# Optimization experiments

Hardware: AMD Instinct MI355X
Metric: run time of the kernel (lower is better)

## Reference

```python
import jax, jax.numpy as jnp
import numpy as np

NV = 100000   # vehicle nodes
NE = 100000   # 'edge' nodes (dst type)
E = 250000    # graph edges (connects relation)
VDIM = 16
EDIM = 16
HID = 128
HEADS = 4
DH = 128      # out_feats per head (GATv2Conv(hid, hid))
EPS = 1e-5
NEG_SLOPE = 0.2


def _layernorm(x, g, b):
    mu = x.mean(-1, keepdims=True)
    var = ((x - mu) ** 2).mean(-1, keepdims=True)
    return (x - mu) * jax.lax.rsqrt(var + EPS) * g + b


def setup_inputs() -> dict:
    key = jax.random.key(0)
    ks = jax.random.split(key, 20)
    s = 0.05
    return {
        "v_feat": jax.random.normal(ks[0], (NV, VDIM), jnp.float32),
        "e_feat": jax.random.normal(ks[1], (NE, EDIM), jnp.float32),
        "Wv": jax.random.normal(ks[2], (VDIM, HID), jnp.float32) * s,
        "bv": jnp.zeros((HID,), jnp.float32),
        "gv": jnp.ones((HID,), jnp.float32),
        "betav": jnp.zeros((HID,), jnp.float32),
        "We": jax.random.normal(ks[3], (EDIM, HID), jnp.float32) * s,
        "be": jnp.zeros((HID,), jnp.float32),
        "ge": jnp.ones((HID,), jnp.float32),
        "betae": jnp.zeros((HID,), jnp.float32),
        "Wsrc": jax.random.normal(ks[4], (HID, HEADS * DH), jnp.float32) * s,
        "bsrc": jnp.zeros((HEADS * DH,), jnp.float32),
        "Wdst": jax.random.normal(ks[5], (HID, HEADS * DH), jnp.float32) * s,
        "bdst": jnp.zeros((HEADS * DH,), jnp.float32),
        "attn": jax.random.normal(ks[6], (HEADS, DH), jnp.float32) * s,
        "Wp": jax.random.normal(ks[7], (HID, HID), jnp.float32) * s,
        "bp": jnp.zeros((HID,), jnp.float32),
        "src": jax.random.randint(ks[8], (E,), 0, NV, jnp.int32),
        "dst": jax.random.randint(ks[9], (E,), 0, NE, jnp.int32),
    }


def reference(v_feat, e_feat, Wv, bv, gv, betav, We, be, ge, betae,
              Wsrc, bsrc, Wdst, bdst, attn, Wp, bp, src, dst):
    # --- node-type encoders: Linear -> ReLU -> LayerNorm ---
    h_v = _layernorm(jax.nn.relu(v_feat @ Wv + bv), gv, betav)      # [NV, HID]
    h_e = _layernorm(jax.nn.relu(e_feat @ We + be), ge, betae)      # [NE, HID]

    # --- GATv2Conv (bipartite: vehicle -> edge), 4 heads ---
    fs = (h_v @ Wsrc + bsrc).reshape(NV, HEADS, DH)                 # src proj
    fd = (h_e @ Wdst + bdst).reshape(NE, HEADS, DH)                 # dst proj
    e = jax.nn.leaky_relu(fs[src] + fd[dst], NEG_SLOPE)             # [E, H, D]
    score = jnp.einsum("ehd,hd->eh", e, attn)                       # [E, H]
    # segment-wise (per-dst-node) softmax over incoming edges
    smax = jax.ops.segment_max(score, dst, num_segments=NE)         # [NE, H]
    ex = jnp.exp(score - smax[dst])
    denom = jax.ops.segment_sum(ex, dst, num_segments=NE)
    alpha = ex / denom[dst]                                         # [E, H]
    out = jax.ops.segment_sum(alpha[:, :, None] * fs[src], dst,
                              num_segments=NE)                      # [NE, H, D]

    # HeteroGraphConv mean-aggregate (single relation -> identity),
    # then mean over heads (edge_out.dim()==3 branch)
    edge_out = out.mean(axis=1)                                     # [NE, HID]

    # feature_proj: Linear -> ReLU -> Dropout(eval: identity)
    return jax.nn.relu(edge_out @ Wp + bp)
```

## Files before the change

kernel.cpp:

```cpp
#include <hip/hip_runtime.h>
#include <hip/hip_bf16.h>
#include <math.h>

#define NV 100000
#define NE_N 100000
#define NEDGE 250000
#define NEG 0.2f
#define LN_EPS 1e-5f

typedef __bf16 bf16_t;
typedef __bf16 bf16x8 __attribute__((ext_vector_type(8)));
typedef float f32x4 __attribute__((ext_vector_type(4)));

__device__ inline unsigned short f2bfu(float f) {
    return __builtin_bit_cast(unsigned short, (__bf16)f);
}
__device__ inline float bfu2f(unsigned short u) {
    return (float)__builtin_bit_cast(__bf16, u);
}
__device__ inline float blo(unsigned w) { return __uint_as_float(w << 16); }
__device__ inline float bhi(unsigned w) { return __uint_as_float(w & 0xffff0000u); }
__device__ inline float lrelu(float x) { return x > 0.f ? x : NEG * x; }
__device__ inline unsigned pk2(float a, float b) {
    return (unsigned)f2bfu(a) | ((unsigned)f2bfu(b) << 16);
}

__global__ __launch_bounds__(256) void prep_kernel(
    const float* __restrict__ Wsrc, const float* __restrict__ Wdst,
    const float* __restrict__ Wp, bf16_t* __restrict__ pS,
    bf16_t* __restrict__ pD, bf16_t* __restrict__ pP)
{
    int t = blockIdx.x * 256 + threadIdx.x;
    if (t < 8192) {
        int ksq = t >> 9, col = t & 511;
#pragma unroll
        for (int j = 0; j < 8; ++j)
            pS[(size_t)t * 8 + j] = (bf16_t)Wsrc[(ksq * 8 + j) * 512 + col];
    } else if (t < 16384) {
        int g = t - 8192;
        int ksq = g >> 9, col = g & 511;
#pragma unroll
        for (int j = 0; j < 8; ++j)
            pD[(size_t)g * 8 + j] = (bf16_t)Wdst[(ksq * 8 + j) * 512 + col];
    } else if (t < 18432) {
        int g = t - 16384;
        int ksq = g >> 7, col = g & 127;
#pragma unroll
        for (int j = 0; j < 8; ++j)
            pP[(size_t)g * 8 + j] = (bf16_t)Wp[(ksq * 8 + j) * 128 + col];
    }
}

__global__ __launch_bounds__(256) void count_kernel(
    const int* __restrict__ dst, int* __restrict__ deg)
{
    int t = blockIdx.x * 256 + threadIdx.x;
    if (t < NEDGE) atomicAdd(&deg[dst[t]], 1);
}

__global__ __launch_bounds__(256) void scan1_kernel(
    const int* __restrict__ deg, int* __restrict__ offs, int* __restrict__ bsum)
{
    __shared__ int s[256];
    int i = blockIdx.x * 256 + threadIdx.x;
    int v = (i < NE_N) ? deg[i] : 0;
    s[threadIdx.x] = v;
    __syncthreads();
    for (int off = 1; off < 256; off <<= 1) {
        int t_ = (threadIdx.x >= off) ? s[threadIdx.x - off] : 0;
        __syncthreads();
        s[threadIdx.x] += t_;
        __syncthreads();
    }
    if (i < NE_N) offs[i] = s[threadIdx.x] - v;
    if (threadIdx.x == 255) bsum[blockIdx.x] = s[255];
}

__global__ __launch_bounds__(512) void scan2_kernel(int* __restrict__ bsum, int nb)
{
    __shared__ int s[512];
    int t = threadIdx.x;
    int v = (t < nb) ? bsum[t] : 0;
    s[t] = v;
    __syncthreads();
    for (int off = 1; off < 512; off <<= 1) {
        int t_ = (t >= off) ? s[t - off] : 0;
        __syncthreads();
        s[t] += t_;
        __syncthreads();
    }
    if (t < nb) bsum[t] = s[t] - v;
}

__global__ __launch_bounds__(256) void scan3_kernel(
    int* __restrict__ offs, const int* __restrict__ bsum, int* __restrict__ cursor)
{
    int i = blockIdx.x * 256 + threadIdx.x;
    if (i < NE_N) {
        int o = offs[i] + bsum[blockIdx.x];
        offs[i] = o;
        cursor[i] = o;
    }
}

__global__ __launch_bounds__(256) void scatter_kernel(
    const int* __restrict__ dst, int* __restrict__ cursor, int* __restrict__ eidx)
{
    int t = blockIdx.x * 256 + threadIdx.x;
    if (t < NEDGE) {
        int pos = atomicAdd(&cursor[dst[t]], 1);
        eidx[pos] = t;
    }
}

__global__ __launch_bounds__(256, 4) void enc_proj_kernel(
    const float* __restrict__ featV, const float* __restrict__ WencV,
    const float* __restrict__ bencV, const float* __restrict__ gV,
    const float* __restrict__ betaV, const bf16_t* __restrict__ ApackV,
    const float* __restrict__ bprojV, unsigned short* __restrict__ outV,
    const float* __restrict__ featE, const float* __restrict__ WencE,
    const float* __restrict__ bencE, const float* __restrict__ gE,
    const float* __restrict__ betaE, const bf16_t* __restrict__ ApackE,
    const float* __restrict__ bprojE, unsigned short* __restrict__ outE,
    int nblk1, int M)
{
    __shared__ unsigned short Hs[64 * 136];

    int b = blockIdx.x;
    bool isV = b < nblk1;
    const float* feat  = isV ? featV  : featE;
    const float* Wenc  = isV ? WencV  : WencE;
    const float* benc  = isV ? bencV  : bencE;
    const float* gln   = isV ? gV     : gE;
    const float* beta  = isV ? betaV  : betaE;
    const bf16_t* Apack = isV ? ApackV : ApackE;
    const float* bproj = isV ? bprojV : bprojE;
    unsigned short* out = isV ? outV : outE;
    int row0 = (isV ? b : b - nblk1) * 64;

    int t = threadIdx.x;
    int l = t & 63;
    int w = t >> 6;
    int rbase = __builtin_amdgcn_readfirstlane(w * 16);

    float wc0[16], wc1[16];
#pragma unroll
    for (int k = 0; k < 16; ++k) {
        float2 wv = *(const float2*)(Wenc + k * 128 + 2 * l);
        wc0[k] = wv.x;
        wc1[k] = wv.y;
    }
    float2 bv2 = *(const float2*)(benc + 2 * l);

#pragma unroll
    for (int i = 0; i < 16; ++i) {
        int grow = row0 + rbase + i;
        if (grow >= M) grow = M - 1;
        const float* fr = feat + (size_t)grow * 16;
        float a0 = bv2.x, a1 = bv2.y;
#pragma unroll
        for (int k = 0; k < 16; ++k) {
            float f = fr[k];
            a0 = fmaf(f, wc0[k], a0);
            a1 = fmaf(f, wc1[k], a1);
        }
        a0 = fmaxf(a0, 0.f);
        a1 = fmaxf(a1, 0.f);
        *(unsigned*)&Hs[(rbase + i) * 136 + 2 * l] = pk2(a0, a1);
    }

    float s = 0.f, s2 = 0.f;
    {
        int rr = rbase + (l >> 2);
        int q = l & 3;
#pragma unroll
        for (int j = 0; j < 4; ++j) {
            uint4 v = *(const uint4*)&Hs[rr * 136 + q * 32 + j * 8];
            float x;
            x = blo(v.x); s += x; s2 = fmaf(x, x, s2);
            x = bhi(v.x); s += x; s2 = fmaf(x, x, s2);
            x = blo(v.y); s += x; s2 = fmaf(x, x, s2);
            x = bhi(v.y); s += x; s2 = fmaf(x, x, s2);
            x = blo(v.z); s += x; s2 = fmaf(x, x, s2);
            x = bhi(v.z); s += x; s2 = fmaf(x, x, s2);
            x = blo(v.w); s += x; s2 = fmaf(x, x, s2);
            x = bhi(v.w); s += x; s2 = fmaf(x, x, s2);
        }
    }
    s  += __shfl_xor(s, 1, 64);  s  += __shfl_xor(s, 2, 64);
    s2 += __shfl_xor(s2, 1, 64); s2 += __shfl_xor(s2, 2, 64);
    float mu  = s * (1.f / 128.f);
    float var = s2 * (1.f / 128.f) - mu * mu;
    float inv = rsqrtf(var + LN_EPS);

    int kq = l >> 4;
    int ln = l & 15;
    float mu_r  = __shfl(mu,  ln * 4, 64);
    float inv_r = __shfl(inv, ln * 4, 64);

    bf16x8 bfr[4];
#pragma unroll
    for (int ks = 0; ks < 4; ++ks) {
        int c0 = ks * 32 + kq * 8;
        uint4 v = *(const uint4*)&Hs[(rbase + ln) * 136 + c0];
        float4 g0 = *(const float4*)(gln + c0);
        float4 g1 = *(const float4*)(gln + c0 + 4);
        float4 b0 = *(const float4*)(beta + c0);
        float4 b1 = *(const float4*)(beta + c0 + 4);
        uint4 p;
        p.x = pk2(fmaf((blo(v.x) - mu_r) * inv_r, g0.x, b0.x),
                  fmaf((bhi(v.x) - mu_r) * inv_r, g0.y, b0.y));
        p.y = pk2(fmaf((blo(v.y) - mu_r) * inv_r, g0.z, b0.z),
                  fmaf((bhi(v.y) - mu_r) * inv_r, g0.w, b0.w));
        p.z = pk2(fmaf((blo(v.z) - mu_r) * inv_r, g1.x, b1.x),
                  fmaf((bhi(v.z) - mu_r) * inv_r, g1.y, b1.y));
        p.w = pk2(fmaf((blo(v.w) - mu_r) * inv_r, g1.z, b1.z),
                  fmaf((bhi(v.w) - mu_r) * inv_r, g1.w, b1.w));
        bfr[ks] = __builtin_bit_cast(bf16x8, p);
    }

    unsigned short* stag = Hs + rbase * 136;
    int node = row0 + rbase + ln;
    bool wr = node < M;

    bf16x8 a_cur[4], a_nxt[4];
#pragma unroll
    for (int ks = 0; ks < 4; ++ks)
        a_cur[ks] = *(const bf16x8*)(Apack + ((size_t)(ks * 4 + kq) * 512 + ln) * 8);

#pragma unroll
    for (int pass = 0; pass < 4; ++pass) {
        int colp = pass * 128;
#pragma unroll
        for (int mt = 0; mt < 8; ++mt) {
            int nidx = pass * 8 + mt + 1;
            if (nidx < 32) {
                int ncol = (nidx >> 3) * 128 + (nidx & 7) * 16 + ln;
#pragma unroll
                for (int ks = 0; ks < 4; ++ks)
                    a_nxt[ks] = *(const bf16x8*)(Apack + ((size_t)(ks * 4 + kq) * 512 + ncol) * 8);
            }

            f32x4 acc = {0.f, 0.f, 0.f, 0.f};
#pragma unroll
            for (int ks = 0; ks < 4; ++ks)
                acc = __builtin_amdgcn_mfma_f32_16x16x32_bf16(a_cur[ks], bfr[ks], acc, 0, 0, 0);

            int col = colp + mt * 16 + kq * 4;
            float4 bb = *(const float4*)(bproj + col);
            ushort4 o;
            o.x = f2bfu(acc[0] + bb.x);
            o.y = f2bfu(acc[1] + bb.y);
            o.z = f2bfu(acc[2] + bb.z);
            o.w = f2bfu(acc[3] + bb.w);
            *(ushort4*)&stag[ln * 136 + mt * 16 + kq * 4] = o;

#pragma unroll
            for (int ks = 0; ks < 4; ++ks)
                a_cur[ks] = a_nxt[ks];
        }
#pragma unroll
        for (int i = 0; i < 4; ++i) {
            uint4 v = *(const uint4*)&stag[ln * 136 + i * 32 + kq * 8];
            if (wr)
                *(uint4*)(out + (size_t)node * 512 + colp + i * 32 + kq * 8) = v;
        }
    }
}

__global__ __launch_bounds__(256) void final_gemm_kernel(
    const float* __restrict__ A, const bf16_t* __restrict__ Ppack,
    const float* __restrict__ bp, float* __restrict__ C, int M)
{
    __shared__ unsigned short Hs[64 * 136];
    int t = threadIdx.x;
    int lane = t & 63;
    int w = t >> 6;
    int row0 = blockIdx.x * 64;

#pragma unroll
    for (int i = 0; i < 8; ++i) {
        int f4 = i * 256 + t;
        int r = f4 >> 5;
        int c4 = (f4 & 31) * 4;
        float4 v = make_float4(0.f, 0.f, 0.f, 0.f);
        if (row0 + r < M)
            v = ((const float4*)(A + (size_t)(row0 + r) * 128))[f4 & 31];
        ushort4 o;
        o.x = f2bfu(v.x); o.y = f2bfu(v.y); o.z = f2bfu(v.z); o.w = f2bfu(v.w);
        *(ushort4*)&Hs[r * 136 + c4] = o;
    }
    __syncthreads();

    int kq = lane >> 4;
    int ln = lane & 15;

    f32x4 acc[2][4];
#pragma unroll
    for (int mt = 0; mt < 2; ++mt)
#pragma unroll
        for (int nt = 0; nt < 4; ++nt) {
            f32x4 z = {0.f, 0.f, 0.f, 0.f};
            acc[mt][nt] = z;
        }

#pragma unroll
    for (int ks = 0; ks < 4; ++ks) {
        bf16x8 bfr[4];
#pragma unroll
        for (int nt = 0; nt < 4; ++nt) {
            const uint4* p = (const uint4*)&Hs[(nt * 16 + ln) * 136 + ks * 32 + kq * 8];
            bfr[nt] = __builtin_bit_cast(bf16x8, *p);
        }
        bf16x8 afr[2];
#pragma unroll
        for (int mt = 0; mt < 2; ++mt) {
            int colA = w * 32 + mt * 16 + ln;
            afr[mt] = *(const bf16x8*)(Ppack + ((size_t)(ks * 4 + kq) * 128 + colA) * 8);
        }
#pragma unroll
        for (int mt = 0; mt < 2; ++mt)
#pragma unroll
            for (int nt = 0; nt < 4; ++nt)
                acc[mt][nt] = __builtin_amdgcn_mfma_f32_16x16x32_bf16(
                    afr[mt], bfr[nt], acc[mt][nt], 0, 0, 0);
    }

#pragma unroll
    for (int mt = 0; mt < 2; ++mt) {
        int col = w * 32 + mt * 16 + kq * 4;
        float4 bb = *(const float4*)(bp + col);
#pragma unroll
        for (int nt = 0; nt < 4; ++nt) {
            int node = row0 + nt * 16 + ln;
            if (node < M) {
                float4 o;
                o.x = fmaxf(acc[mt][nt][0] + bb.x, 0.f);
                o.y = fmaxf(acc[mt][nt][1] + bb.y, 0.f);
                o.z = fmaxf(acc[mt][nt][2] + bb.z, 0.f);
                o.w = fmaxf(acc[mt][nt][3] + bb.w, 0.f);
                *(float4*)(C + (size_t)node * 128 + col) = o;
            }
        }
    }
}

__global__ __launch_bounds__(256) void softagg_kernel(
    const unsigned short* __restrict__ fs, const unsigned short* __restrict__ fdp,
    const float* __restrict__ attn, const int* __restrict__ src,
    const int* __restrict__ offs, const int* __restrict__ deg,
    const int* __restrict__ eidx, float* __restrict__ out)
{
    int d = blockIdx.x * 4 + (threadIdx.x >> 6);
    if (d >= NE_N) return;
    int l = threadIdx.x & 63;
    int r0 = offs[d];
    int n = deg[d];
    int o = l * 8;

    uint4 fv = *(const uint4*)(fdp + (size_t)d * 512 + o);
    float fdv[8] = { blo(fv.x), bhi(fv.x), blo(fv.y), bhi(fv.y),
                     blo(fv.z), bhi(fv.z), blo(fv.w), bhi(fv.w) };
    float4 w0 = *(const float4*)(attn + o);
    float4 w1 = *(const float4*)(attn + o + 4);
    float wv[8] = { w0.x, w0.y, w0.z, w0.w, w1.x, w1.y, w1.z, w1.w };

    float m = -1e30f, sm = 0.f;
    float acc[8];
#pragma unroll
    for (int j = 0; j < 8; ++j) acc[j] = 0.f;

    for (int base = 0; base < n; base += 64) {
        int cnt = min(n - base, 64);
        int sl = 0;
        if (l < cnt) sl = src[eidx[r0 + base + l]];
        for (int i = 0; i < cnt; ++i) {
            int s = __shfl(sl, i, 64);
            uint4 a = *(const uint4*)(fs + (size_t)s * 512 + o);
            float fsv[8] = { blo(a.x), bhi(a.x), blo(a.y), bhi(a.y),
                             blo(a.z), bhi(a.z), blo(a.w), bhi(a.w) };
            float p = 0.f;
#pragma unroll
            for (int j = 0; j < 8; ++j)
                p = fmaf(lrelu(fsv[j] + fdv[j]), wv[j], p);
#pragma unroll
            for (int mk = 1; mk < 16; mk <<= 1)
                p += __shfl_xor(p, mk, 64);
            float mn = fmaxf(m, p);
            float c  = __expf(m - mn);
            float av = __expf(p - mn);
            sm = sm * c + av;
            m = mn;
#pragma unroll
            for (int j = 0; j < 8; ++j)
                acc[j] = fmaf(av, fsv[j], acc[j] * c);
        }
    }

    float inv = (n > 0) ? 0.25f / sm : 0.f;
#pragma unroll
    for (int j = 0; j < 8; ++j) {
        float v = acc[j] * inv;
        v += __shfl_xor(v, 16, 64);
        v += __shfl_xor(v, 32, 64);
        acc[j] = v;
    }
    if (l < 16) {
        float4 o0 = make_float4(acc[0], acc[1], acc[2], acc[3]);
        float4 o1 = make_float4(acc[4], acc[5], acc[6], acc[7]);
        *(float4*)(out + (size_t)d * 128 + l * 8) = o0;
        *(float4*)(out + (size_t)d * 128 + l * 8 + 4) = o1;
    }
}

extern "C" void kernel_launch(void* const* d_in, const int* in_sizes, int n_in,
                              void* d_out, int out_size, void* d_ws, size_t ws_size,
                              hipStream_t stream)
{
    const float* v_feat = (const float*)d_in[0];
    const float* e_feat = (const float*)d_in[1];
    const float* Wv     = (const float*)d_in[2];
    const float* bv     = (const float*)d_in[3];
    const float* gv     = (const float*)d_in[4];
    const float* betav  = (const float*)d_in[5];
    const float* We     = (const float*)d_in[6];
    const float* be     = (const float*)d_in[7];
    const float* ge     = (const float*)d_in[8];
    const float* betae  = (const float*)d_in[9];
    const float* Wsrc   = (const float*)d_in[10];
    const float* bsrc   = (const float*)d_in[11];
    const float* Wdst   = (const float*)d_in[12];
    const float* bdst   = (const float*)d_in[13];
    const float* attn   = (const float*)d_in[14];
    const float* Wp     = (const float*)d_in[15];
    const float* bp     = (const float*)d_in[16];
    const int*   src    = (const int*)d_in[17];
    const int*   dst    = (const int*)d_in[18];
    float* out = (float*)d_out;

    unsigned short* fs = (unsigned short*)d_ws;
    unsigned short* fd = fs + (size_t)NV * 512;
    int* deg    = (int*)(fd + (size_t)NE_N * 512);
    int* offs   = deg + NE_N;
    int* cursor = offs + NE_N;
    int* bsum   = cursor + NE_N;
    int* eidx   = bsum + 512;
    bf16_t* pS  = (bf16_t*)(eidx + NEDGE);
    bf16_t* pD  = pS + 65536;
    bf16_t* pP  = pD + 65536;

    const int NB_SCAN = (NE_N + 255) / 256;

    prep_kernel<<<72, 256, 0, stream>>>(Wsrc, Wdst, Wp, pS, pD, pP);

    hipMemsetAsync(deg, 0, (size_t)NE_N * sizeof(int), stream);
    count_kernel<<<(NEDGE + 255) / 256, 256, 0, stream>>>(dst, deg);
    scan1_kernel<<<NB_SCAN, 256, 0, stream>>>(deg, offs, bsum);
    scan2_kernel<<<1, 512, 0, stream>>>(bsum, NB_SCAN);
    scan3_kernel<<<NB_SCAN, 256, 0, stream>>>(offs, bsum, cursor);
    scatter_kernel<<<(NEDGE + 255) / 256, 256, 0, stream>>>(dst, cursor, eidx);

    enc_proj_kernel<<<3126, 256, 0, stream>>>(
        v_feat, Wv, bv, gv, betav, pS, bsrc, fs,
        e_feat, We, be, ge, betae, pD, bdst, fd,
        1563, 100000);

    softagg_kernel<<<NE_N / 4, 256, 0, stream>>>(fs, fd, attn, src, offs, deg,
                                                 eidx, out);

    final_gemm_kernel<<<1563, 256, 0, stream>>>(out, pP, bp, out, NE_N);
}
```

Measured before the change: 334.8 us.

## Restructure encoder-projection kernel to single-wave blocks processing 32 rows each

The encoder+projection kernel changes from 4-wave blocks, where each wave handles 16 rows, to 1-wave blocks where the wave handles 32 rows as two 16-row MFMA tiles. Each loaded weight fragment (Apack) now feeds two MFMAs, halving the weight-fragment global loads per row, and the LayerNorm reduction is reorganised to two lanes per row. The trade-off is more blocks, fewer waves per block, more registers per wave (two B-fragment sets and accumulators), and a longer serial encoder loop per wave, which may reduce latency hiding.

```diff
diff --git a/kernel.cpp b/kernel.cpp
--- a/kernel.cpp
+++ b/kernel.cpp
@@ -113,7 +113,7 @@
     }
 }
 
-__global__ __launch_bounds__(256, 4) void enc_proj_kernel(
+__global__ __launch_bounds__(64, 4) void enc_proj_kernel(
     const float* __restrict__ featV, const float* __restrict__ WencV,
     const float* __restrict__ bencV, const float* __restrict__ gV,
     const float* __restrict__ betaV, const bf16_t* __restrict__ ApackV,
@@ -124,24 +124,21 @@
     const float* __restrict__ bprojE, unsigned short* __restrict__ outE,
     int nblk1, int M)
 {
-    __shared__ unsigned short Hs[64 * 136];
+    __shared__ unsigned short Hs[32 * 136];
 
     int b = blockIdx.x;
     bool isV = b < nblk1;
-    const float* feat  = isV ? featV  : featE;
-    const float* Wenc  = isV ? WencV  : WencE;
-    const float* benc  = isV ? bencV  : bencE;
-    const float* gln   = isV ? gV     : gE;
-    const float* beta  = isV ? betaV  : betaE;
+    const float* feat   = isV ? featV  : featE;
+    const float* Wenc   = isV ? WencV  : WencE;
+    const float* benc   = isV ? bencV  : bencE;
+    const float* gln    = isV ? gV     : gE;
+    const float* beta   = isV ? betaV  : betaE;
     const bf16_t* Apack = isV ? ApackV : ApackE;
-    const float* bproj = isV ? bprojV : bprojE;
+    const float* bproj  = isV ? bprojV : bprojE;
     unsigned short* out = isV ? outV : outE;
-    int row0 = (isV ? b : b - nblk1) * 64;
-
-    int t = threadIdx.x;
-    int l = t & 63;
-    int w = t >> 6;
-    int rbase = __builtin_amdgcn_readfirstlane(w * 16);
+    int row0 = (isV ? b : b - nblk1) * 32;
+
+    int l = threadIdx.x;
 
     float wc0[16], wc1[16];
 #pragma unroll
@@ -153,8 +150,8 @@
     float2 bv2 = *(const float2*)(benc + 2 * l);
 
 #pragma unroll
-    for (int i = 0; i < 16; ++i) {
-        int grow = row0 + rbase + i;
+    for (int i = 0; i < 32; ++i) {
+        int grow = row0 + i;
         if (grow >= M) grow = M - 1;
         const float* fr = feat + (size_t)grow * 16;
         float a0 = bv2.x, a1 = bv2.y;
@@ -166,16 +163,16 @@
         }
         a0 = fmaxf(a0, 0.f);
         a1 = fmaxf(a1, 0.f);
-        *(unsigned*)&Hs[(rbase + i) * 136 + 2 * l] = pk2(a0, a1);
+        *(unsigned*)&Hs[i * 136 + 2 * l] = pk2(a0, a1);
     }
 
     float s = 0.f, s2 = 0.f;
     {
-        int rr = rbase + (l >> 2);
-        int q = l & 3;
-#pragma unroll
-        for (int j = 0; j < 4; ++j) {
-            uint4 v = *(const uint4*)&Hs[rr * 136 + q * 32 + j * 8];
+        int rr = l >> 1;
+        int h = l & 1;
+#pragma unroll
+        for (int j = 0; j < 8; ++j) {
+            uint4 v = *(const uint4*)&Hs[rr * 136 + h * 64 + j * 8];
             float x;
             x = blo(v.x); s += x; s2 = fmaf(x, x, s2);
             x = bhi(v.x); s += x; s2 = fmaf(x, x, s2);
@@ -187,41 +184,49 @@
             x = bhi(v.w); s += x; s2 = fmaf(x, x, s2);
         }
     }
-    s  += __shfl_xor(s, 1, 64);  s  += __shfl_xor(s, 2, 64);
-    s2 += __shfl_xor(s2, 1, 64); s2 += __shfl_xor(s2, 2, 64);
+    s  += __shfl_xor(s, 1, 64);
+    s2 += __shfl_xor(s2, 1, 64);
     float mu  = s * (1.f / 128.f);
     float var = s2 * (1.f / 128.f) - mu * mu;
     float inv = rsqrtf(var + LN_EPS);
 
     int kq = l >> 4;
     int ln = l & 15;
-    float mu_r  = __shfl(mu,  ln * 4, 64);
-    float inv_r = __shfl(inv, ln * 4, 64);
-
-    bf16x8 bfr[4];
+    float mu0  = __shfl(mu,  ln * 2, 64);
+    float inv0 = __shfl(inv, ln * 2, 64);
+    float mu1  = __shfl(mu,  (16 + ln) * 2, 64);
+    float inv1 = __shfl(inv, (16 + ln) * 2, 64);
+
+    bf16x8 bfr[2][4];
 #pragma unroll
     for (int ks = 0; ks < 4; ++ks) {
         int c0 = ks * 32 + kq * 8;
-        uint4 v = *(const uint4*)&Hs[(rbase + ln) * 136 + c0];
         float4 g0 = *(const float4*)(gln + c0);
         float4 g1 = *(const float4*)(gln + c0 + 4);
         float4 b0 = *(const float4*)(beta + c0);
         float4 b1 = *(const float4*)(beta + c0 + 4);
-        uint4 p;
-        p.x = pk2(fmaf((blo(v.x) - mu_r) * inv_r, g0.x, b0.x),
-                  fmaf((bhi(v.x) - mu_r) * inv_r, g0.y, b0.y));
-        p.y = pk2(fmaf((blo(v.y) - mu_r) * inv_r, g0.z, b0.z),
-                  fmaf((bhi(v.y) - mu_r) * inv_r, g0.w, b0.w));
-        p.z = pk2(fmaf((blo(v.z) - mu_r) * inv_r, g1.x, b1.x),
-                  fmaf((bhi(v.z) - mu_r) * inv_r, g1.y, b1.y));
-        p.w = pk2(fmaf((blo(v.w) - mu_r) * inv_r, g1.z, b1.z),
-                  fmaf((bhi(v.w) - mu_r) * inv_r, g1.w, b1.w));
-        bfr[ks] = __builtin_bit_cast(bf16x8, p);
-    }
-
-    unsigned short* stag = Hs + rbase * 136;
-    int node = row0 + rbase + ln;
-    bool wr = node < M;
+#pragma unroll
+        for (int nt = 0; nt < 2; ++nt) {
+            float m_ = nt ? mu1 : mu0;
+            float i_ = nt ? inv1 : inv0;
+            uint4 v = *(const uint4*)&Hs[(nt * 16 + ln) * 136 + c0];
+            uint4 p;
+            p.x = pk2(fmaf((blo(v.x) - m_) * i_, g0.x, b0.x),
+                      fmaf((bhi(v.x) - m_) * i_, g0.y, b0.y));
+            p.y = pk2(fmaf((blo(v.y) - m_) * i_, g0.z, b0.z),
+                      fmaf((bhi(v.y) - m_) * i_, g0.w, b0.w));
+            p.z = pk2(fmaf((blo(v.z) - m_) * i_, g1.x, b1.x),
+                      fmaf((bhi(v.z) - m_) * i_, g1.y, b1.y));
+            p.w = pk2(fmaf((blo(v.w) - m_) * i_, g1.z, b1.z),
+                      fmaf((bhi(v.w) - m_) * i_, g1.w, b1.w));
+            bfr[nt][ks] = __builtin_bit_cast(bf16x8, p);
+        }
+    }
+
+    int node0 = row0 + ln;
+    int node1 = row0 + 16 + ln;
+    bool wr0 = node0 < M;
+    bool wr1 = node1 < M;
 
     bf16x8 a_cur[4], a_nxt[4];
 #pragma unroll
@@ -235,25 +240,29 @@
         for (int mt = 0; mt < 8; ++mt) {
             int nidx = pass * 8 + mt + 1;
             if (nidx < 32) {
-                int ncol = (nidx >> 3) * 128 + (nidx & 7) * 16 + ln;
+                int ncol = nidx * 16 + ln;
 #pragma unroll
                 for (int ks = 0; ks < 4; ++ks)
                     a_nxt[ks] = *(const bf16x8*)(Apack + ((size_t)(ks * 4 + kq) * 512 + ncol) * 8);
             }
 
-            f32x4 acc = {0.f, 0.f, 0.f, 0.f};
-#pragma unroll
-            for (int ks = 0; ks < 4; ++ks)
-                acc = __builtin_amdgcn_mfma_f32_16x16x32_bf16(a_cur[ks], bfr[ks], acc, 0, 0, 0);
+            f32x4 acc0 = {0.f, 0.f, 0.f, 0.f};
+            f32x4 acc1 = {0.f, 0.f, 0.f, 0.f};
+#pragma unroll
+            for (int ks = 0; ks < 4; ++ks) {
+                acc0 = __builtin_amdgcn_mfma_f32_16x16x32_bf16(a_cur[ks], bfr[0][ks], acc0, 0, 0, 0);
+                acc1 = __builtin_amdgcn_mfma_f32_16x16x32_bf16(a_cur[ks], bfr[1][ks], acc1, 0, 0, 0);
+            }
 
             int col = colp + mt * 16 + kq * 4;
             float4 bb = *(const float4*)(bproj + col);
-            ushort4 o;
-            o.x = f2bfu(acc[0] + bb.x);
-            o.y = f2bfu(acc[1] + bb.y);
-            o.z = f2bfu(acc[2] + bb.z);
-            o.w = f2bfu(acc[3] + bb.w);
-            *(ushort4*)&stag[ln * 136 + mt * 16 + kq * 4] = o;
+            ushort4 o0, o1;
+            o0.x = f2bfu(acc0[0] + bb.x); o0.y = f2bfu(acc0[1] + bb.y);
+            o0.z = f2bfu(acc0[2] + bb.z); o0.w = f2bfu(acc0[3] + bb.w);
+            o1.x = f2bfu(acc1[0] + bb.x); o1.y = f2bfu(acc1[1] + bb.y);
+            o1.z = f2bfu(acc1[2] + bb.z); o1.w = f2bfu(acc1[3] + bb.w);
+            *(ushort4*)&Hs[ln * 136 + mt * 16 + kq * 4] = o0;
+            *(ushort4*)&Hs[(16 + ln) * 136 + mt * 16 + kq * 4] = o1;
 
 #pragma unroll
             for (int ks = 0; ks < 4; ++ks)
@@ -261,9 +270,12 @@
         }
 #pragma unroll
         for (int i = 0; i < 4; ++i) {
-            uint4 v = *(const uint4*)&stag[ln * 136 + i * 32 + kq * 8];
-            if (wr)
-                *(uint4*)(out + (size_t)node * 512 + colp + i * 32 + kq * 8) = v;
+            uint4 v0 = *(const uint4*)&Hs[ln * 136 + i * 32 + kq * 8];
+            if (wr0)
+                *(uint4*)(out + (size_t)node0 * 512 + colp + i * 32 + kq * 8) = v0;
+            uint4 v1 = *(const uint4*)&Hs[(16 + ln) * 136 + i * 32 + kq * 8];
+            if (wr1)
+                *(uint4*)(out + (size_t)node1 * 512 + colp + i * 32 + kq * 8) = v1;
         }
     }
 }
@@ -460,10 +472,10 @@
     scan3_kernel<<<NB_SCAN, 256, 0, stream>>>(offs, bsum, cursor);
     scatter_kernel<<<(NEDGE + 255) / 256, 256, 0, stream>>>(dst, cursor, eidx);
 
-    enc_proj_kernel<<<3126, 256, 0, stream>>>(
+    enc_proj_kernel<<<6250, 64, 0, stream>>>(
         v_feat, Wv, bv, gv, betav, pS, bsrc, fs,
         e_feat, We, be, ge, betae, pD, bdst, fd,
-        1563, 100000);
+        3125, 100000);
 
     softagg_kernel<<<NE_N / 4, 256, 0, stream>>>(fs, fd, attn, src, offs, deg,
                                                  eidx, out);
```

Measured after the change: 335.4 us. No clear change (+0.2%).
